# Optimization experiments

Measured on AMD Instinct MI355X. Metric: run time of the kernel, lower is better.

## Reference

```python
import jax, jax.numpy as jnp
import numpy as np

B, T, F = 8, 8192, 1024
H, O = 256, 2


def setup_inputs() -> dict:
    key = jax.random.key(0)
    ks = jax.random.split(key, 12)
    s = 0.02
    return {
        "bags": jax.random.normal(ks[0], (B, T, F), dtype=jnp.float32),
        "mask": jnp.zeros((B, T), dtype=bool),
        "W1": jax.random.normal(ks[1], (F, H), dtype=jnp.float32) * s,
        "b1": jnp.zeros((H,), dtype=jnp.float32),
        "Wv": jax.random.normal(ks[2], (H, H), dtype=jnp.float32) * s,
        "bv": jnp.zeros((H,), dtype=jnp.float32),
        "Wu": jax.random.normal(ks[3], (H, H), dtype=jnp.float32) * s,
        "bu": jnp.zeros((H,), dtype=jnp.float32),
        "ww": jax.random.normal(ks[4], (H, 1), dtype=jnp.float32) * s,
        "bw": jnp.zeros((1,), dtype=jnp.float32),
        "Wc": jax.random.normal(ks[5], (H, O), dtype=jnp.float32) * s,
        "bc": jnp.zeros((O,), dtype=jnp.float32),
    }


def reference(bags, mask, W1, b1, Wv, bv, Wu, bu, ww, bw, Wc, bc):
    # Feature projection + ReLU (dropout is identity in eval mode)
    h = jax.nn.relu(jnp.einsum("btf,fh->bth", bags, W1) + b1)  # (B,T,H)
    # Gated attention
    a_v = jnp.tanh(jnp.einsum("bth,hk->btk", h, Wv) + bv)
    a_u = jax.nn.sigmoid(jnp.einsum("bth,hk->btk", h, Wu) + bu)
    attn_logits = (jnp.einsum("bth,ho->bto", a_v * a_u, ww) + bw)[..., 0]  # (B,T)
    attn_logits = jnp.where(mask, -jnp.inf, attn_logits)
    attn = jax.nn.softmax(attn_logits, axis=1)  # (B,T)
    # Weighted aggregation over tiles
    slide_repr = jnp.einsum("bt,bth->bh", attn, h)  # (B,H)
    logits = slide_repr @ Wc + bc  # (B,O)
    return logits
```

## Files before the change

kernel.cpp:

```cpp
#include <hip/hip_runtime.h>
#include <math.h>

#define BB 8
#define TT 8192
#define FF 1024
#define HH 256
#define MT 64
#define NBLK ((BB*TT)/MT)
#define PBAG (TT/MT)
#define PSTR 260

typedef __attribute__((ext_vector_type(8))) short bf16x8;
typedef __attribute__((ext_vector_type(4))) float f32x4;

__device__ __forceinline__ float b2f(unsigned short s) {
    union { unsigned u; float f; } v; v.u = ((unsigned)s) << 16; return v.f;
}
__device__ __forceinline__ unsigned short f2b(float f) {
    union { float f; unsigned u; } v; v.f = f;
    unsigned u = v.u;
    return (unsigned short)((u + 0x7fffu + ((u >> 16) & 1u)) >> 16);
}
__device__ __forceinline__ unsigned pk2(float a, float b) {
    return (unsigned)f2b(a) | ((unsigned)f2b(b) << 16);
}

__global__ __launch_bounds__(256)
void mil_prep(const float* __restrict__ W1,
              const float* __restrict__ Wv,
              const float* __restrict__ Wu,
              unsigned short* __restrict__ W1f,
              unsigned short* __restrict__ Wvf,
              unsigned short* __restrict__ Wuf) {
    __shared__ unsigned short T[64 * 264];
    const int b = blockIdx.x;
    const int t = threadIdx.x;
    if (b < 64) {
        const int w = b >> 4, kb = b & 15;
#pragma unroll
        for (int i = 0; i < 4; ++i) {
            int f = t + i * 256;
            int r = f >> 4, c4 = (f & 15) * 4;
            float4 v = *(const float4*)(W1 + (size_t)(kb * 64 + r) * 256 + w * 64 + c4);
            T[(c4 + 0) * 72 + r] = f2b(v.x);
            T[(c4 + 1) * 72 + r] = f2b(v.y);
            T[(c4 + 2) * 72 + r] = f2b(v.z);
            T[(c4 + 3) * 72 + r] = f2b(v.w);
        }
        __syncthreads();
#pragma unroll
        for (int i = 0; i < 2; ++i) {
            int c = t + i * 256;
            int fl = c >> 6;
            int k0i = fl >> 2, ni = fl & 3;
            int lane = c & 63, l15 = lane & 15, q = lane >> 4;
            *(uint4*)(W1f + ((size_t)(w * 16 + kb) * 8 + fl) * 512 + lane * 8) =
                *(const uint4*)&T[(ni * 16 + l15) * 72 + k0i * 32 + q * 8];
        }
    } else {
        const int m = (b - 64) >> 2;
        const int w = (b - 64) & 3;
        const float* src = m ? Wu : Wv;
        unsigned short* dst = m ? Wuf : Wvf;
#pragma unroll
        for (int i = 0; i < 16; ++i) {
            int f = t + i * 256;
            int r = f >> 4, c4 = (f & 15) * 4;
            float4 v = *(const float4*)(src + (size_t)r * 256 + w * 64 + c4);
            T[(c4 + 0) * 264 + r] = f2b(v.x);
            T[(c4 + 1) * 264 + r] = f2b(v.y);
            T[(c4 + 2) * 264 + r] = f2b(v.z);
            T[(c4 + 3) * 264 + r] = f2b(v.w);
        }
        __syncthreads();
#pragma unroll
        for (int i = 0; i < 8; ++i) {
            int c = t + i * 256;
            int fl = c >> 6;
            int nc = fl >> 3, ks = fl & 7;
            int lane = c & 63, l15 = lane & 15, q = lane >> 4;
            *(uint4*)(dst + ((size_t)(w * 4 + nc) * 8 + ks) * 512 + lane * 8) =
                *(const uint4*)&T[(nc * 16 + l15) * 264 + ks * 32 + q * 8];
        }
    }
}

__global__ __launch_bounds__(256, 2)
void mil_stage1(const float* __restrict__ bags,
                const float* __restrict__ b1,
                const unsigned short* __restrict__ W1f,
                unsigned short* __restrict__ Hg) {
    const int tid  = threadIdx.x;
    const int wave = tid >> 6;
    const int lane = tid & 63;
    const int l15  = lane & 15;
    const int quad = lane >> 4;
    const int blk  = blockIdx.x;

    __shared__ unsigned short LB[2 * 64 * 136];

    f32x4 acc[4][4];
#pragma unroll
    for (int mi = 0; mi < 4; ++mi)
#pragma unroll
        for (int ni = 0; ni < 4; ++ni)
            acc[mi][ni] = (f32x4){0.f, 0.f, 0.f, 0.f};

    const float* bagrow = bags + (size_t)blk * MT * FF;
    int fr[8], fc[8];
    float4 pf[8];
#pragma unroll
    for (int i = 0; i < 8; ++i) {
        int f = tid + i * 256;
        fr[i] = f >> 5;
        fc[i] = (f & 31) * 4;
        pf[i] = *(const float4*)(bagrow + (size_t)fr[i] * FF + fc[i]);
    }
    const unsigned short* bs = W1f + (size_t)wave * 16 * 4096;

#pragma unroll 2
    for (int kb2 = 0; kb2 < 8; ++kb2) {
        unsigned short* A = LB + (kb2 & 1) * 8704;
#pragma unroll
        for (int i = 0; i < 8; ++i)
            *(uint2*)&A[fr[i] * 136 + fc[i]] =
                make_uint2(pk2(pf[i].x, pf[i].y), pk2(pf[i].z, pf[i].w));
        __syncthreads();
        bf16x8 bb[16];
#pragma unroll
        for (int f16 = 0; f16 < 16; ++f16)
            bb[f16] = *(const bf16x8*)(bs + (size_t)(kb2 * 2 + (f16 >> 3)) * 4096
                                       + (f16 & 7) * 512 + lane * 8);
        if (kb2 < 7) {
#pragma unroll
            for (int i = 0; i < 8; ++i)
                pf[i] = *(const float4*)(bagrow + (size_t)fr[i] * FF + (kb2 + 1) * 128 + fc[i]);
        }
#pragma unroll
        for (int k0i = 0; k0i < 4; ++k0i) {
            bf16x8 afr[4];
#pragma unroll
            for (int mi = 0; mi < 4; ++mi)
                afr[mi] = *(const bf16x8*)&A[(mi * 16 + l15) * 136 + k0i * 32 + quad * 8];
#pragma unroll
            for (int mi = 0; mi < 4; ++mi)
#pragma unroll
                for (int ni = 0; ni < 4; ++ni)
                    acc[mi][ni] = __builtin_amdgcn_mfma_f32_16x16x32_bf16(afr[mi], bb[k0i * 4 + ni], acc[mi][ni], 0, 0, 0);
        }
    }
    __syncthreads();

    {
        float bbv[4];
#pragma unroll
        for (int ni = 0; ni < 4; ++ni) bbv[ni] = b1[wave * 64 + ni * 16 + l15];
#pragma unroll
        for (int mi = 0; mi < 4; ++mi)
#pragma unroll
            for (int ni = 0; ni < 4; ++ni) {
                int n = wave * 64 + ni * 16 + l15;
#pragma unroll
                for (int r = 0; r < 4; ++r) {
                    int m = mi * 16 + quad * 4 + r;
                    float h = fmaxf(acc[mi][ni][r] + bbv[ni], 0.f);
                    LB[m * 264 + n] = f2b(h);
                }
            }
    }
    __syncthreads();
#pragma unroll
    for (int i = 0; i < 8; ++i) {
        int f = tid + i * 256;
        int r = f >> 5, c8 = (f & 31) * 8;
        *(uint4*)(Hg + (size_t)blk * 16384 + r * 256 + c8) = *(const uint4*)&LB[r * 264 + c8];
    }
}

__global__ __launch_bounds__(256, 4)
void mil_stage2(const unsigned short* __restrict__ Hg,
                const unsigned char* __restrict__ mask,
                const float* __restrict__ bv,
                const float* __restrict__ bu,
                const float* __restrict__ ww,
                const float* __restrict__ bwp,
                const unsigned short* __restrict__ Wvf,
                const unsigned short* __restrict__ Wuf,
                float* __restrict__ P) {
    const int tid  = threadIdx.x;
    const int wave = tid >> 6;
    const int lane = tid & 63;
    const int l15  = lane & 15;
    const int quad = lane >> 4;
    const int blk  = blockIdx.x;
    const int bag  = blk >> 7;
    const int trow = (blk & 127) * MT;

    __shared__ unsigned short Hs[MT * 264];
    __shared__ float logits[MT];
    __shared__ float wrow[MT];
    __shared__ float sc[2];

#pragma unroll
    for (int i = 0; i < 8; ++i) {
        int f = tid + i * 256;
        int r = f >> 5, c8 = (f & 31) * 8;
        *(uint4*)&Hs[r * 264 + c8] = *(const uint4*)(Hg + (size_t)blk * 16384 + r * 256 + c8);
    }
    if (tid < MT) logits[tid] = 0.f;
    __syncthreads();

    float rsum[4][4];
#pragma unroll
    for (int mi = 0; mi < 4; ++mi)
#pragma unroll
        for (int r = 0; r < 4; ++r) rsum[mi][r] = 0.f;

#pragma unroll 1
    for (int nc = 0; nc < 4; ++nc) {
        const int n = wave * 64 + nc * 16 + l15;
        const unsigned short* vs = Wvf + ((size_t)(wave * 4 + nc) * 8) * 512;
        const unsigned short* us = Wuf + ((size_t)(wave * 4 + nc) * 8) * 512;
        f32x4 av[4], au[4];
#pragma unroll
        for (int mi = 0; mi < 4; ++mi) {
            av[mi] = (f32x4){0.f, 0.f, 0.f, 0.f};
            au[mi] = (f32x4){0.f, 0.f, 0.f, 0.f};
        }
#pragma unroll 2
        for (int ks = 0; ks < 8; ++ks) {
            bf16x8 bvf = *(const bf16x8*)(vs + ks * 512 + lane * 8);
            bf16x8 buf_ = *(const bf16x8*)(us + ks * 512 + lane * 8);
            bf16x8 afr[4];
#pragma unroll
            for (int mi = 0; mi < 4; ++mi)
                afr[mi] = *(const bf16x8*)&Hs[(mi * 16 + l15) * 264 + ks * 32 + quad * 8];
#pragma unroll
            for (int mi = 0; mi < 4; ++mi) {
                av[mi] = __builtin_amdgcn_mfma_f32_16x16x32_bf16(afr[mi], bvf, av[mi], 0, 0, 0);
                au[mi] = __builtin_amdgcn_mfma_f32_16x16x32_bf16(afr[mi], buf_, au[mi], 0, 0, 0);
            }
        }
        const float bvn = bv[n], bun = bu[n], wn = ww[n];
#pragma unroll
        for (int mi = 0; mi < 4; ++mi)
#pragma unroll
            for (int r = 0; r < 4; ++r) {
                float xv = av[mi][r] + bvn;
                float xu = au[mi][r] + bun;
                float tv = 2.f * __frcp_rn(1.f + __expf(-2.f * xv)) - 1.f;
                float su = __frcp_rn(1.f + __expf(-xu));
                rsum[mi][r] += tv * su * wn;
            }
    }
#pragma unroll
    for (int mi = 0; mi < 4; ++mi)
#pragma unroll
        for (int r = 0; r < 4; ++r) {
            float s = rsum[mi][r];
            s += __shfl_xor(s, 1);
            s += __shfl_xor(s, 2);
            s += __shfl_xor(s, 4);
            s += __shfl_xor(s, 8);
            if (l15 == 0) atomicAdd(&logits[mi * 16 + quad * 4 + r], s);
        }
    __syncthreads();

    if (tid < MT) {
        float lg = logits[tid] + bwp[0];
        if (mask[bag * TT + trow + tid]) lg = -INFINITY;
        logits[tid] = lg;
    }
    __syncthreads();

    if (wave == 0) {
        float v = logits[lane];
        float mx = v;
#pragma unroll
        for (int off = 1; off < 64; off <<= 1) mx = fmaxf(mx, __shfl_xor(mx, off));
        float w = (mx == -INFINITY) ? 0.f : __expf(v - mx);
        wrow[lane] = w;
        float l = w;
#pragma unroll
        for (int off = 1; off < 64; off <<= 1) l += __shfl_xor(l, off);
        if (lane == 0) { sc[0] = mx; sc[1] = l; }
    }
    __syncthreads();

    float a = 0.f;
#pragma unroll 8
    for (int m = 0; m < MT; ++m)
        a += wrow[m] * b2f(Hs[m * 264 + tid]);

    float* rec = P + (size_t)blk * PSTR;
    rec[2 + tid] = a;
    if (tid == 0) { rec[0] = sc[0]; rec[1] = sc[1]; }
}

__global__ void mil_final(const float* __restrict__ P,
                          const float* __restrict__ Wc,
                          const float* __restrict__ bc,
                          float* __restrict__ out) {
    const int bag = blockIdx.x;
    const int tid = threadIdx.x;
    __shared__ float marr[PBAG];
    __shared__ float earr[PBAG];
    __shared__ float red[4];
    __shared__ float wred[8];

    if (tid < PBAG) marr[tid] = P[(size_t)(bag * PBAG + tid) * PSTR + 0];
    __syncthreads();
    if (tid < PBAG) {
        float v = marr[tid];
#pragma unroll
        for (int off = 1; off < 64; off <<= 1) v = fmaxf(v, __shfl_xor(v, off));
        if ((tid & 63) == 0) red[tid >> 6] = v;
    }
    __syncthreads();
    const float M = fmaxf(red[0], red[1]);
    if (tid < PBAG) {
        float e = (marr[tid] == -INFINITY) ? 0.f : __expf(marr[tid] - M);
        earr[tid] = e;
        float le = P[(size_t)(bag * PBAG + tid) * PSTR + 1] * e;
#pragma unroll
        for (int off = 1; off < 64; off <<= 1) le += __shfl_xor(le, off);
        if ((tid & 63) == 0) red[2 + (tid >> 6)] = le;
    }
    __syncthreads();
    const float L = red[2] + red[3];

    float accv = 0.f;
#pragma unroll 4
    for (int i = 0; i < PBAG; ++i)
        accv += earr[i] * P[(size_t)(bag * PBAG + i) * PSTR + 2 + tid];
    const float sr = accv / L;

    float p0 = sr * Wc[tid * 2 + 0];
    float p1 = sr * Wc[tid * 2 + 1];
#pragma unroll
    for (int off = 1; off < 64; off <<= 1) {
        p0 += __shfl_xor(p0, off);
        p1 += __shfl_xor(p1, off);
    }
    if ((tid & 63) == 0) {
        wred[(tid >> 6) * 2 + 0] = p0;
        wred[(tid >> 6) * 2 + 1] = p1;
    }
    __syncthreads();
    if (tid == 0) {
        out[bag * 2 + 0] = wred[0] + wred[2] + wred[4] + wred[6] + bc[0];
        out[bag * 2 + 1] = wred[1] + wred[3] + wred[5] + wred[7] + bc[1];
    }
}

extern "C" void kernel_launch(void* const* d_in, const int* in_sizes, int n_in,
                              void* d_out, int out_size, void* d_ws, size_t ws_size,
                              hipStream_t stream) {
    const float*         bags = (const float*)d_in[0];
    const unsigned char* mask = (const unsigned char*)d_in[1];
    const float*         W1   = (const float*)d_in[2];
    const float*         b1   = (const float*)d_in[3];
    const float*         Wv   = (const float*)d_in[4];
    const float*         bv   = (const float*)d_in[5];
    const float*         Wu   = (const float*)d_in[6];
    const float*         bu   = (const float*)d_in[7];
    const float*         ww   = (const float*)d_in[8];
    const float*         bw   = (const float*)d_in[9];
    const float*         Wc   = (const float*)d_in[10];
    const float*         bc   = (const float*)d_in[11];
    float* out = (float*)d_out;

    char* ws = (char*)d_ws;
    unsigned short* W1f = (unsigned short*)(ws);
    unsigned short* Wvf = (unsigned short*)(ws + 524288);
    unsigned short* Wuf = (unsigned short*)(ws + 655360);
    float*          P   = (float*)(ws + 786432);
    unsigned short* Hg  = (unsigned short*)(ws + 1851392);

    mil_prep<<<72, 256, 0, stream>>>(W1, Wv, Wu, W1f, Wvf, Wuf);
    mil_stage1<<<NBLK, 256, 0, stream>>>(bags, b1, W1f, Hg);
    mil_stage2<<<NBLK, 256, 0, stream>>>(Hg, mask, bv, bu, ww, bw, Wvf, Wuf, P);
    mil_final<<<BB, 256, 0, stream>>>(P, Wc, bc, out);
}
```

Measured before the change: 444.9 us.

## Fuse feature projection and gated attention into one kernel keeping H in LDS

Merges stage1 (bags×W1 + ReLU) and stage2 (gated attention, local softmax, weighted sum) into a single kernel. The bf16 hidden tile stays in shared memory instead of being written to and reread from a global buffer, which also removes one launch. In exchange the fused kernel runs at the stage1 occupancy bound (2 blocks per CU) and carries the combined register pressure of both phases.

```diff
diff --git a/kernel.cpp b/kernel.cpp
--- a/kernel.cpp
+++ b/kernel.cpp
@@ -86,107 +86,17 @@
 }
 
 __global__ __launch_bounds__(256, 2)
-void mil_stage1(const float* __restrict__ bags,
-                const float* __restrict__ b1,
-                const unsigned short* __restrict__ W1f,
-                unsigned short* __restrict__ Hg) {
-    const int tid  = threadIdx.x;
-    const int wave = tid >> 6;
-    const int lane = tid & 63;
-    const int l15  = lane & 15;
-    const int quad = lane >> 4;
-    const int blk  = blockIdx.x;
-
-    __shared__ unsigned short LB[2 * 64 * 136];
-
-    f32x4 acc[4][4];
-#pragma unroll
-    for (int mi = 0; mi < 4; ++mi)
-#pragma unroll
-        for (int ni = 0; ni < 4; ++ni)
-            acc[mi][ni] = (f32x4){0.f, 0.f, 0.f, 0.f};
-
-    const float* bagrow = bags + (size_t)blk * MT * FF;
-    int fr[8], fc[8];
-    float4 pf[8];
-#pragma unroll
-    for (int i = 0; i < 8; ++i) {
-        int f = tid + i * 256;
-        fr[i] = f >> 5;
-        fc[i] = (f & 31) * 4;
-        pf[i] = *(const float4*)(bagrow + (size_t)fr[i] * FF + fc[i]);
-    }
-    const unsigned short* bs = W1f + (size_t)wave * 16 * 4096;
-
-#pragma unroll 2
-    for (int kb2 = 0; kb2 < 8; ++kb2) {
-        unsigned short* A = LB + (kb2 & 1) * 8704;
-#pragma unroll
-        for (int i = 0; i < 8; ++i)
-            *(uint2*)&A[fr[i] * 136 + fc[i]] =
-                make_uint2(pk2(pf[i].x, pf[i].y), pk2(pf[i].z, pf[i].w));
-        __syncthreads();
-        bf16x8 bb[16];
-#pragma unroll
-        for (int f16 = 0; f16 < 16; ++f16)
-            bb[f16] = *(const bf16x8*)(bs + (size_t)(kb2 * 2 + (f16 >> 3)) * 4096
-                                       + (f16 & 7) * 512 + lane * 8);
-        if (kb2 < 7) {
-#pragma unroll
-            for (int i = 0; i < 8; ++i)
-                pf[i] = *(const float4*)(bagrow + (size_t)fr[i] * FF + (kb2 + 1) * 128 + fc[i]);
-        }
-#pragma unroll
-        for (int k0i = 0; k0i < 4; ++k0i) {
-            bf16x8 afr[4];
-#pragma unroll
-            for (int mi = 0; mi < 4; ++mi)
-                afr[mi] = *(const bf16x8*)&A[(mi * 16 + l15) * 136 + k0i * 32 + quad * 8];
-#pragma unroll
-            for (int mi = 0; mi < 4; ++mi)
-#pragma unroll
-                for (int ni = 0; ni < 4; ++ni)
-                    acc[mi][ni] = __builtin_amdgcn_mfma_f32_16x16x32_bf16(afr[mi], bb[k0i * 4 + ni], acc[mi][ni], 0, 0, 0);
-        }
-    }
-    __syncthreads();
-
-    {
-        float bbv[4];
-#pragma unroll
-        for (int ni = 0; ni < 4; ++ni) bbv[ni] = b1[wave * 64 + ni * 16 + l15];
-#pragma unroll
-        for (int mi = 0; mi < 4; ++mi)
-#pragma unroll
-            for (int ni = 0; ni < 4; ++ni) {
-                int n = wave * 64 + ni * 16 + l15;
-#pragma unroll
-                for (int r = 0; r < 4; ++r) {
-                    int m = mi * 16 + quad * 4 + r;
-                    float h = fmaxf(acc[mi][ni][r] + bbv[ni], 0.f);
-                    LB[m * 264 + n] = f2b(h);
-                }
-            }
-    }
-    __syncthreads();
-#pragma unroll
-    for (int i = 0; i < 8; ++i) {
-        int f = tid + i * 256;
-        int r = f >> 5, c8 = (f & 31) * 8;
-        *(uint4*)(Hg + (size_t)blk * 16384 + r * 256 + c8) = *(const uint4*)&LB[r * 264 + c8];
-    }
-}
-
-__global__ __launch_bounds__(256, 4)
-void mil_stage2(const unsigned short* __restrict__ Hg,
-                const unsigned char* __restrict__ mask,
-                const float* __restrict__ bv,
-                const float* __restrict__ bu,
-                const float* __restrict__ ww,
-                const float* __restrict__ bwp,
-                const unsigned short* __restrict__ Wvf,
-                const unsigned short* __restrict__ Wuf,
-                float* __restrict__ P) {
+void mil_fused(const float* __restrict__ bags,
+               const float* __restrict__ b1,
+               const unsigned short* __restrict__ W1f,
+               const unsigned char* __restrict__ mask,
+               const float* __restrict__ bv,
+               const float* __restrict__ bu,
+               const float* __restrict__ ww,
+               const float* __restrict__ bwp,
+               const unsigned short* __restrict__ Wvf,
+               const unsigned short* __restrict__ Wuf,
+               float* __restrict__ P) {
     const int tid  = threadIdx.x;
     const int wave = tid >> 6;
     const int lane = tid & 63;
@@ -196,16 +106,79 @@
     const int bag  = blk >> 7;
     const int trow = (blk & 127) * MT;
 
-    __shared__ unsigned short Hs[MT * 264];
+    __shared__ unsigned short LB[2 * 64 * 136];
     __shared__ float logits[MT];
     __shared__ float wrow[MT];
     __shared__ float sc[2];
 
+    f32x4 acc[4][4];
+#pragma unroll
+    for (int mi = 0; mi < 4; ++mi)
+#pragma unroll
+        for (int ni = 0; ni < 4; ++ni)
+            acc[mi][ni] = (f32x4){0.f, 0.f, 0.f, 0.f};
+
+    const float* bagrow = bags + (size_t)blk * MT * FF;
+    int fr[8], fc[8];
+    float4 pf[8];
 #pragma unroll
     for (int i = 0; i < 8; ++i) {
         int f = tid + i * 256;
-        int r = f >> 5, c8 = (f & 31) * 8;
-        *(uint4*)&Hs[r * 264 + c8] = *(const uint4*)(Hg + (size_t)blk * 16384 + r * 256 + c8);
+        fr[i] = f >> 5;
+        fc[i] = (f & 31) * 4;
+        pf[i] = *(const float4*)(bagrow + (size_t)fr[i] * FF + fc[i]);
+    }
+    const unsigned short* bs = W1f + (size_t)wave * 16 * 4096;
+
+#pragma unroll 2
+    for (int kb2 = 0; kb2 < 8; ++kb2) {
+        unsigned short* A = LB + (kb2 & 1) * 8704;
+#pragma unroll
+        for (int i = 0; i < 8; ++i)
+            *(uint2*)&A[fr[i] * 136 + fc[i]] =
+                make_uint2(pk2(pf[i].x, pf[i].y), pk2(pf[i].z, pf[i].w));
+        __syncthreads();
+        bf16x8 bb[16];
+#pragma unroll
+        for (int f16 = 0; f16 < 16; ++f16)
+            bb[f16] = *(const bf16x8*)(bs + (size_t)(kb2 * 2 + (f16 >> 3)) * 4096
+                                       + (f16 & 7) * 512 + lane * 8);
+        if (kb2 < 7) {
+#pragma unroll
+            for (int i = 0; i < 8; ++i)
+                pf[i] = *(const float4*)(bagrow + (size_t)fr[i] * FF + (kb2 + 1) * 128 + fc[i]);
+        }
+#pragma unroll
+        for (int k0i = 0; k0i < 4; ++k0i) {
+            bf16x8 afr[4];
+#pragma unroll
+            for (int mi = 0; mi < 4; ++mi)
+                afr[mi] = *(const bf16x8*)&A[(mi * 16 + l15) * 136 + k0i * 32 + quad * 8];
+#pragma unroll
+            for (int mi = 0; mi < 4; ++mi)
+#pragma unroll
+                for (int ni = 0; ni < 4; ++ni)
+                    acc[mi][ni] = __builtin_amdgcn_mfma_f32_16x16x32_bf16(afr[mi], bb[k0i * 4 + ni], acc[mi][ni], 0, 0, 0);
+        }
+    }
+    __syncthreads();
+
+    {
+        float bbv[4];
+#pragma unroll
+        for (int ni = 0; ni < 4; ++ni) bbv[ni] = b1[wave * 64 + ni * 16 + l15];
+#pragma unroll
+        for (int mi = 0; mi < 4; ++mi)
+#pragma unroll
+            for (int ni = 0; ni < 4; ++ni) {
+                int n = wave * 64 + ni * 16 + l15;
+#pragma unroll
+                for (int r = 0; r < 4; ++r) {
+                    int m = mi * 16 + quad * 4 + r;
+                    float h = fmaxf(acc[mi][ni][r] + bbv[ni], 0.f);
+                    LB[m * 264 + n] = f2b(h);
+                }
+            }
     }
     if (tid < MT) logits[tid] = 0.f;
     __syncthreads();
@@ -234,7 +207,7 @@
             bf16x8 afr[4];
 #pragma unroll
             for (int mi = 0; mi < 4; ++mi)
-                afr[mi] = *(const bf16x8*)&Hs[(mi * 16 + l15) * 264 + ks * 32 + quad * 8];
+                afr[mi] = *(const bf16x8*)&LB[(mi * 16 + l15) * 264 + ks * 32 + quad * 8];
 #pragma unroll
             for (int mi = 0; mi < 4; ++mi) {
                 av[mi] = __builtin_amdgcn_mfma_f32_16x16x32_bf16(afr[mi], bvf, av[mi], 0, 0, 0);
@@ -290,7 +263,7 @@
     float a = 0.f;
 #pragma unroll 8
     for (int m = 0; m < MT; ++m)
-        a += wrow[m] * b2f(Hs[m * 264 + tid]);
+        a += wrow[m] * b2f(LB[m * 264 + tid]);
 
     float* rec = P + (size_t)blk * PSTR;
     rec[2 + tid] = a;
@@ -375,10 +348,8 @@
     unsigned short* Wvf = (unsigned short*)(ws + 524288);
     unsigned short* Wuf = (unsigned short*)(ws + 655360);
     float*          P   = (float*)(ws + 786432);
-    unsigned short* Hg  = (unsigned short*)(ws + 1851392);
 
     mil_prep<<<72, 256, 0, stream>>>(W1, Wv, Wu, W1f, Wvf, Wuf);
-    mil_stage1<<<NBLK, 256, 0, stream>>>(bags, b1, W1f, Hg);
-    mil_stage2<<<NBLK, 256, 0, stream>>>(Hg, mask, bv, bu, ww, bw, Wvf, Wuf, P);
+    mil_fused<<<NBLK, 256, 0, stream>>>(bags, b1, W1f, mask, bv, bu, ww, bw, Wvf, Wuf, P);
     mil_final<<<BB, 256, 0, stream>>>(P, Wc, bc, out);
 }
```

Measured after the change: 430.6 us. 1.03x faster.
